# Optimization experiments

Measured on AMD Instinct MI355X. Metric: run time of the kernel, lower is better.

The kernel has to match this reference:

```python
import jax, jax.numpy as jnp
import numpy as np

S_MIN, S_MAX, ALPHA = 1, 5, 5.0
EPS = 1e-6


def _conv2d_same(x, k):
    # x: [B,1,H,W], k: [1,1,3,3], stride 1, padding 1
    return jax.lax.conv_general_dilated(x, k, (1, 1), ((1, 1), (1, 1)),
                                        dimension_numbers=('NCHW', 'OIHW', 'NCHW'))


def sobel_complexity(x):
    # compute_spatial_complexity_sobel: per-image min-max normalized gradient magnitude
    xg = x.mean(1, keepdims=True)  # [B,1,H,W]
    sx = jnp.array([[1, 0, -1], [2, 0, -2], [1, 0, -1]], x.dtype).reshape(1, 1, 3, 3)
    sy = jnp.array([[1, 2, 1], [0, 0, 0], [-1, -2, -1]], x.dtype).reshape(1, 1, 3, 3)
    gx = _conv2d_same(xg, sx)
    gy = _conv2d_same(xg, sy)
    mag = jnp.sqrt(gx ** 2 + gy ** 2 + EPS)
    mn = mag.min((2, 3), keepdims=True)
    mx = mag.max((2, 3), keepdims=True)
    rng = mx - mn
    c = jnp.where(rng > 0, (mag - mn) / (rng + EPS), jnp.zeros_like(mag))
    return c[:, 0]  # [B,H,W]


def adaptive_steps(m):
    # adaptive_step_from_complexity, fully vectorized
    B, H, W = m.shape
    avg = jnp.ones((1, 1, 3, 3), m.dtype) / 9.0
    lc = _conv2d_same(m[:, None], avg)[:, 0]  # [B,H,W] local complexity
    hm, wm = H // 2, W // 2
    rc = jnp.stack([m[:, :hm, :wm].mean((1, 2)), m[:, :hm, wm:].mean((1, 2)),
                    m[:, hm:, :wm].mean((1, 2)), m[:, hm:, wm:].mean((1, 2))], axis=1)  # [B,4]
    base = S_MAX - jax.nn.sigmoid(ALPHA * (rc - 0.5)) * (S_MAX - S_MIN)
    base = jnp.round(jnp.clip(base, S_MIN, S_MAX)).astype(jnp.int32)  # [B,4]
    adj = jnp.round(jax.nn.sigmoid(ALPHA * (lc - 0.5)) * 2.0 - 1.0).astype(jnp.int32)  # [B,H,W]
    return jnp.clip(base[:, :, None, None] + adj[:, None], S_MIN, S_MAX)  # [B,4,H,W]


def _visits_lr(step):
    # step: [B,R,L] int. Left-to-right adaptive-step traversal along last axis per row.
    # Returns float mask [B,R,L] of visited positions.
    B, R, L = step.shape
    s = jnp.maximum(step, 1)

    def body(j, _):
        valid = j < L                       # [B,R]
        jc = jnp.minimum(j, L - 1)
        st = jnp.take_along_axis(s, jc[:, :, None], -1)[:, :, 0]
        return jnp.where(valid, j + st, j), (jc, valid)

    _, (jcs, valids) = jax.lax.scan(body, jnp.zeros((B, R), jnp.int32), None, length=L)
    jcs = jnp.moveaxis(jcs, 0, -1)          # [B,R,L]
    valids = jnp.moveaxis(valids, 0, -1)    # [B,R,L]
    bi = jnp.arange(B)[:, None, None]
    ri = jnp.arange(R)[None, :, None]
    vis = jnp.zeros((B, R, L), jnp.float32).at[bi, ri, jcs].add(valids.astype(jnp.float32))
    return (vis > 0).astype(jnp.float32)


def _visits_rl(step):
    # Right-to-left traversal == left-to-right on the mirrored step map, mirrored back.
    return jnp.flip(_visits_lr(jnp.flip(step, -1)), -1)


def _forward(x):
    m = sobel_complexity(x)                 # [B,H,W]
    steps = adaptive_steps(m)               # [B,4,H,W]
    v0 = _visits_lr(steps[:, 0])            # rows, left->right
    v1 = _visits_rl(steps[:, 1])            # rows, right->left
    v2 = jnp.swapaxes(_visits_lr(jnp.swapaxes(steps[:, 2], 1, 2)), 1, 2)  # cols, top->down
    v3 = jnp.swapaxes(_visits_rl(jnp.swapaxes(steps[:, 3], 1, 2)), 1, 2)  # cols, bottom->up
    V = v0 + v1 + v2 + v3                   # [B,H,W] visit counts
    # DirectionalScan followed by DirectionalMerge: output = sum_d x*visit_d / (V + 1e-6)
    return x * (V / (V + 1e-6))[:, None]


def setup_inputs() -> dict:
    key = jax.random.key(0)
    x = jax.random.normal(key, (8, 96, 256, 256), dtype=jnp.float32)
    return {"x": x}


def reference(x):
    return _forward(x)
```

## Files before the change

### kernel.cpp

```cpp
#include <hip/hip_runtime.h>
#include <math.h>

#define BB 8
#define CC 96
#define HH 256
#define WW 256
#define HW (HH*WW)

typedef unsigned long long u64;

__global__ void k_init(unsigned* mn_u, unsigned* mx_u) {
    int t = threadIdx.x;
    if (t < BB) { mn_u[t] = 0x7f800000u; mx_u[t] = 0u; }
}

__global__ void k_mean(const float* __restrict__ x, float* __restrict__ m) {
    int i = blockIdx.x * blockDim.x + threadIdx.x;
    const int per = HW / 4;
    if (i >= BB * per) return;
    int b = i / per, hw4 = i % per;
    const float4* xb = reinterpret_cast<const float4*>(x) + (size_t)b * CC * per + hw4;
    double a0 = 0, a1 = 0, a2 = 0, a3 = 0;
    for (int c = 0; c < CC; ++c) {
        float4 v = xb[(size_t)c * per];
        a0 += (double)v.x; a1 += (double)v.y; a2 += (double)v.z; a3 += (double)v.w;
    }
    float4 o;
    o.x = (float)(a0 / 96.0); o.y = (float)(a1 / 96.0);
    o.z = (float)(a2 / 96.0); o.w = (float)(a3 / 96.0);
    reinterpret_cast<float4*>(m)[i] = o;
}

__global__ void k_sobel(const float* __restrict__ m, float* __restrict__ mag,
                        unsigned* mn_u, unsigned* mx_u) {
    int row = blockIdx.x;
    int b = row >> 8, h = row & 255, w = threadIdx.x;
    const float* mb = m + (size_t)b * HW;
    auto at = [&](int hh, int ww) -> float {
        if (hh < 0 || hh >= HH || ww < 0 || ww >= WW) return 0.0f;
        return mb[hh * WW + ww];
    };
    float a00 = at(h - 1, w - 1), a01 = at(h - 1, w), a02 = at(h - 1, w + 1);
    float a10 = at(h, w - 1),                         a12 = at(h, w + 1);
    float a20 = at(h + 1, w - 1), a21 = at(h + 1, w), a22 = at(h + 1, w + 1);
    float gx = a00 - a02 + 2.0f * a10 - 2.0f * a12 + a20 - a22;
    float gy = a00 + 2.0f * a01 + a02 - a20 - 2.0f * a21 - a22;
    float mg = sqrtf(gx * gx + gy * gy + 1e-6f);
    mag[row * WW + w] = mg;

    float lmn = mg, lmx = mg;
    for (int off = 32; off; off >>= 1) {
        lmn = fminf(lmn, __shfl_down(lmn, off));
        lmx = fmaxf(lmx, __shfl_down(lmx, off));
    }
    __shared__ float smn[4], smx[4];
    int wv = threadIdx.x >> 6, ln = threadIdx.x & 63;
    if (ln == 0) { smn[wv] = lmn; smx[wv] = lmx; }
    __syncthreads();
    if (threadIdx.x == 0) {
        float bmn = fminf(fminf(smn[0], smn[1]), fminf(smn[2], smn[3]));
        float bmx = fmaxf(fmaxf(smx[0], smx[1]), fmaxf(smx[2], smx[3]));
        atomicMin(&mn_u[b], __float_as_uint(bmn));
        atomicMax(&mx_u[b], __float_as_uint(bmx));
    }
}

__global__ void k_cnorm(const float* __restrict__ mag, const unsigned* __restrict__ mn_u,
                        const unsigned* __restrict__ mx_u, float* __restrict__ c,
                        float* __restrict__ part) {
    int row = blockIdx.x;
    int b = row >> 8, w = threadIdx.x;
    float mn = __uint_as_float(mn_u[b]);
    float mx = __uint_as_float(mx_u[b]);
    float rng = mx - mn;
    float mg = mag[row * WW + w];
    float cc = (rng > 0.0f) ? (mg - mn) / (rng + 1e-6f) : 0.0f;
    c[row * WW + w] = cc;

    float r = cc;
    for (int off = 32; off; off >>= 1) r += __shfl_down(r, off);
    __shared__ float s[4];
    int wv = threadIdx.x >> 6, ln = threadIdx.x & 63;
    if (ln == 0) s[wv] = r;
    __syncthreads();
    if (threadIdx.x == 0) {
        part[row * 2 + 0] = s[0] + s[1];
        part[row * 2 + 1] = s[2] + s[3];
    }
}

__global__ void k_base(const float* __restrict__ part, int* __restrict__ base) {
    int t = threadIdx.x;
    if (t >= 32) return;
    int b = t >> 2, q = t & 3;
    int hlo = (q >> 1) ? 128 : 0;
    int col = q & 1;
    double s = 0.0;
    for (int h = hlo; h < hlo + 128; ++h) s += (double)part[(b * HH + h) * 2 + col];
    float rc = (float)(s / 16384.0);
    float sig = 1.0f / (1.0f + expf(-5.0f * (rc - 0.5f)));
    float bs = 5.0f - sig * 4.0f;
    bs = fminf(fmaxf(bs, 1.0f), 5.0f);
    base[b * 4 + q] = (int)rintf(bs);
}

__global__ void k_adj(const float* __restrict__ c, signed char* __restrict__ adj) {
    int row = blockIdx.x;
    int b = row >> 8, h = row & 255, w = threadIdx.x;
    const float* cb = c + (size_t)b * HW;
    auto at = [&](int hh, int ww) -> float {
        if (hh < 0 || hh >= HH || ww < 0 || ww >= WW) return 0.0f;
        return cb[hh * WW + ww];
    };
    const float w9 = 1.0f / 9.0f;
    float acc = 0.0f;
    acc = fmaf(at(h - 1, w - 1), w9, acc);
    acc = fmaf(at(h - 1, w    ), w9, acc);
    acc = fmaf(at(h - 1, w + 1), w9, acc);
    acc = fmaf(at(h    , w - 1), w9, acc);
    acc = fmaf(at(h    , w    ), w9, acc);
    acc = fmaf(at(h    , w + 1), w9, acc);
    acc = fmaf(at(h + 1, w - 1), w9, acc);
    acc = fmaf(at(h + 1, w    ), w9, acc);
    acc = fmaf(at(h + 1, w + 1), w9, acc);
    float sg = 1.0f / (1.0f + expf(-5.0f * (acc - 0.5f)));
    adj[row * WW + w] = (signed char)(int)rintf(sg * 2.0f - 1.0f);
}

#define SETBIT(j) do { int _j = (j); \
    if (_j < 64) m0 |= 1ull << _j; \
    else if (_j < 128) m1 |= 1ull << (_j - 64); \
    else if (_j < 192) m2 |= 1ull << (_j - 128); \
    else m3 |= 1ull << (_j - 192); } while (0)

__global__ void k_trav(const signed char* __restrict__ adj, const int* __restrict__ base,
                       u64* __restrict__ masks) {
    int tid = blockIdx.x * blockDim.x + threadIdx.x;
    int dir = tid >> 11;
    int idx = tid & 2047;
    int b = idx >> 8, r = idx & 255;
    int bs = base[b * 4 + dir];
    const signed char* ab = adj + (size_t)b * HW;
    u64 m0 = 0, m1 = 0, m2 = 0, m3 = 0;
    if (dir == 0) {
        int j = 0;
        while (j < WW) {
            SETBIT(j);
            int st = bs + (int)ab[r * WW + j];
            st = st < 1 ? 1 : (st > 5 ? 5 : st);
            j += st;
        }
    } else if (dir == 1) {
        int j = WW - 1;
        while (j >= 0) {
            SETBIT(j);
            int st = bs + (int)ab[r * WW + j];
            st = st < 1 ? 1 : (st > 5 ? 5 : st);
            j -= st;
        }
    } else if (dir == 2) {
        int j = 0;
        while (j < HH) {
            SETBIT(j);
            int st = bs + (int)ab[j * WW + r];
            st = st < 1 ? 1 : (st > 5 ? 5 : st);
            j += st;
        }
    } else {
        int j = HH - 1;
        while (j >= 0) {
            SETBIT(j);
            int st = bs + (int)ab[j * WW + r];
            st = st < 1 ? 1 : (st > 5 ? 5 : st);
            j -= st;
        }
    }
    u64* o = masks + ((size_t)dir * BB * 256 + idx) * 4;
    o[0] = m0; o[1] = m1; o[2] = m2; o[3] = m3;
}

__global__ void k_scale(const u64* __restrict__ masks, float* __restrict__ scale) {
    int row = blockIdx.x;
    int b = row >> 8, h = row & 255, w = threadIdx.x;
    const u64* m0 = masks + (((size_t)0 * BB + b) * 256 + h) * 4;
    const u64* m1 = masks + (((size_t)1 * BB + b) * 256 + h) * 4;
    const u64* m2 = masks + (((size_t)2 * BB + b) * 256 + w) * 4;
    const u64* m3 = masks + (((size_t)3 * BB + b) * 256 + w) * 4;
    int v = (int)((m0[w >> 6] >> (w & 63)) & 1ull)
          + (int)((m1[w >> 6] >> (w & 63)) & 1ull)
          + (int)((m2[h >> 6] >> (h & 63)) & 1ull)
          + (int)((m3[h >> 6] >> (h & 63)) & 1ull);
    float fV = (float)v;
    scale[row * WW + w] = fV / (fV + 1e-6f);
}

__global__ void k_out(const float* __restrict__ x, const float* __restrict__ scale,
                      float* __restrict__ out) {
    const int total4 = BB * CC * HW / 4;
    const int per_img4 = CC * HW / 4;
    const int hw4n = HW / 4;
    const float4* x4 = reinterpret_cast<const float4*>(x);
    const float4* s4 = reinterpret_cast<const float4*>(scale);
    float4* o4 = reinterpret_cast<float4*>(out);
    for (int i = blockIdx.x * blockDim.x + threadIdx.x; i < total4;
         i += gridDim.x * blockDim.x) {
        int b = i / per_img4;
        int hw4 = i % hw4n;
        float4 sv = s4[b * hw4n + hw4];
        float4 xv = x4[i];
        float4 ov;
        ov.x = xv.x * sv.x; ov.y = xv.y * sv.y; ov.z = xv.z * sv.z; ov.w = xv.w * sv.w;
        o4[i] = ov;
    }
}

extern "C" void kernel_launch(void* const* d_in, const int* in_sizes, int n_in,
                              void* d_out, int out_size, void* d_ws, size_t ws_size,
                              hipStream_t stream) {
    const float* x = (const float*)d_in[0];
    float* out = (float*)d_out;
    char* ws = (char*)d_ws;

    float* m     = (float*)(ws);
    float* mag   = (float*)(ws + (size_t)2 * 1024 * 1024);
    float* c     = (float*)(ws + (size_t)4 * 1024 * 1024);
    float* scale = (float*)(ws + (size_t)6 * 1024 * 1024);
    signed char* adj = (signed char*)(ws + (size_t)8 * 1024 * 1024);
    u64* masks   = (u64*)(ws + (size_t)8 * 1024 * 1024 + 524288);
    float* part  = (float*)(ws + (size_t)8 * 1024 * 1024 + 524288 + 262144);
    unsigned* mn_u = (unsigned*)(ws + (size_t)8 * 1024 * 1024 + 524288 + 262144 + 16384);
    unsigned* mx_u = mn_u + 8;
    int* base = (int*)(mn_u + 16);

    k_init<<<1, 64, 0, stream>>>(mn_u, mx_u);
    k_mean<<<(BB * HW / 4 + 255) / 256, 256, 0, stream>>>(x, m);
    k_sobel<<<BB * HH, 256, 0, stream>>>(m, mag, mn_u, mx_u);
    k_cnorm<<<BB * HH, 256, 0, stream>>>(mag, mn_u, mx_u, c, part);
    k_base<<<1, 32, 0, stream>>>(part, base);
    k_adj<<<BB * HH, 256, 0, stream>>>(c, adj);
    k_trav<<<32, 256, 0, stream>>>(adj, base, masks);
    k_scale<<<BB * HH, 256, 0, stream>>>(masks, scale);
    k_out<<<4096, 256, 0, stream>>>(x, scale, out);
}
```

Baseline: 200.8 us.

## Fuse init, normalization, box filter and base-step kernels to cut launches

Folds the min/max init into the mean kernel and merges the normalization and box-filter kernels. The normalized complexity is now recomputed on the fly from the gradient magnitude instead of being stored and reloaded. The base-step computation moves into the traversal kernel as a per-block shared-memory reduction, and the mean loop gets an unroll pragma. This removes three launches and one intermediate buffer, at the cost of redundant divides per stencil tap. The mean kernel dominates the runtime, so the overall effect should be small.

New measurement: 188.2 us. 6.3% less time.

```diff
diff --git a/kernel.cpp b/kernel.cpp
--- a/kernel.cpp
+++ b/kernel.cpp
@@ -9,18 +9,19 @@
 
 typedef unsigned long long u64;
 
-__global__ void k_init(unsigned* mn_u, unsigned* mx_u) {
-    int t = threadIdx.x;
-    if (t < BB) { mn_u[t] = 0x7f800000u; mx_u[t] = 0u; }
-}
-
-__global__ void k_mean(const float* __restrict__ x, float* __restrict__ m) {
+__global__ void k_mean(const float* __restrict__ x, float* __restrict__ m,
+                       unsigned* __restrict__ mn_u, unsigned* __restrict__ mx_u) {
+    if (blockIdx.x == 0 && threadIdx.x < 2 * BB) {
+        if (threadIdx.x < BB) mn_u[threadIdx.x] = 0x7f800000u;
+        else                  mx_u[threadIdx.x - BB] = 0u;
+    }
     int i = blockIdx.x * blockDim.x + threadIdx.x;
     const int per = HW / 4;
     if (i >= BB * per) return;
     int b = i / per, hw4 = i % per;
     const float4* xb = reinterpret_cast<const float4*>(x) + (size_t)b * CC * per + hw4;
     double a0 = 0, a1 = 0, a2 = 0, a3 = 0;
+#pragma unroll 8
     for (int c = 0; c < CC; ++c) {
         float4 v = xb[(size_t)c * per];
         a0 += (double)v.x; a1 += (double)v.y; a2 += (double)v.z; a3 += (double)v.w;
@@ -65,17 +66,21 @@
     }
 }
 
-__global__ void k_cnorm(const float* __restrict__ mag, const unsigned* __restrict__ mn_u,
-                        const unsigned* __restrict__ mx_u, float* __restrict__ c,
-                        float* __restrict__ part) {
+__global__ void k_adjpart(const float* __restrict__ mag, const unsigned* __restrict__ mn_u,
+                          const unsigned* __restrict__ mx_u, signed char* __restrict__ adj,
+                          float* __restrict__ part) {
     int row = blockIdx.x;
-    int b = row >> 8, w = threadIdx.x;
+    int b = row >> 8, h = row & 255, w = threadIdx.x;
     float mn = __uint_as_float(mn_u[b]);
     float mx = __uint_as_float(mx_u[b]);
     float rng = mx - mn;
-    float mg = mag[row * WW + w];
-    float cc = (rng > 0.0f) ? (mg - mn) / (rng + 1e-6f) : 0.0f;
-    c[row * WW + w] = cc;
+    const float* gb = mag + (size_t)b * HW;
+    auto cat = [&](int hh, int ww) -> float {
+        if (hh < 0 || hh >= HH || ww < 0 || ww >= WW) return 0.0f;
+        float mg = gb[hh * WW + ww];
+        return (rng > 0.0f) ? (mg - mn) / (rng + 1e-6f) : 0.0f;
+    };
+    float cc = cat(h, w);
 
     float r = cc;
     for (int off = 32; off; off >>= 1) r += __shfl_down(r, off);
@@ -87,42 +92,18 @@
         part[row * 2 + 0] = s[0] + s[1];
         part[row * 2 + 1] = s[2] + s[3];
     }
-}
-
-__global__ void k_base(const float* __restrict__ part, int* __restrict__ base) {
-    int t = threadIdx.x;
-    if (t >= 32) return;
-    int b = t >> 2, q = t & 3;
-    int hlo = (q >> 1) ? 128 : 0;
-    int col = q & 1;
-    double s = 0.0;
-    for (int h = hlo; h < hlo + 128; ++h) s += (double)part[(b * HH + h) * 2 + col];
-    float rc = (float)(s / 16384.0);
-    float sig = 1.0f / (1.0f + expf(-5.0f * (rc - 0.5f)));
-    float bs = 5.0f - sig * 4.0f;
-    bs = fminf(fmaxf(bs, 1.0f), 5.0f);
-    base[b * 4 + q] = (int)rintf(bs);
-}
-
-__global__ void k_adj(const float* __restrict__ c, signed char* __restrict__ adj) {
-    int row = blockIdx.x;
-    int b = row >> 8, h = row & 255, w = threadIdx.x;
-    const float* cb = c + (size_t)b * HW;
-    auto at = [&](int hh, int ww) -> float {
-        if (hh < 0 || hh >= HH || ww < 0 || ww >= WW) return 0.0f;
-        return cb[hh * WW + ww];
-    };
+
     const float w9 = 1.0f / 9.0f;
     float acc = 0.0f;
-    acc = fmaf(at(h - 1, w - 1), w9, acc);
-    acc = fmaf(at(h - 1, w    ), w9, acc);
-    acc = fmaf(at(h - 1, w + 1), w9, acc);
-    acc = fmaf(at(h    , w - 1), w9, acc);
-    acc = fmaf(at(h    , w    ), w9, acc);
-    acc = fmaf(at(h    , w + 1), w9, acc);
-    acc = fmaf(at(h + 1, w - 1), w9, acc);
-    acc = fmaf(at(h + 1, w    ), w9, acc);
-    acc = fmaf(at(h + 1, w + 1), w9, acc);
+    acc = fmaf(cat(h - 1, w - 1), w9, acc);
+    acc = fmaf(cat(h - 1, w    ), w9, acc);
+    acc = fmaf(cat(h - 1, w + 1), w9, acc);
+    acc = fmaf(cat(h    , w - 1), w9, acc);
+    acc = fmaf(cc,               w9, acc);
+    acc = fmaf(cat(h    , w + 1), w9, acc);
+    acc = fmaf(cat(h + 1, w - 1), w9, acc);
+    acc = fmaf(cat(h + 1, w    ), w9, acc);
+    acc = fmaf(cat(h + 1, w + 1), w9, acc);
     float sg = 1.0f / (1.0f + expf(-5.0f * (acc - 0.5f)));
     adj[row * WW + w] = (signed char)(int)rintf(sg * 2.0f - 1.0f);
 }
@@ -133,13 +114,33 @@
     else if (_j < 192) m2 |= 1ull << (_j - 128); \
     else m3 |= 1ull << (_j - 192); } while (0)
 
-__global__ void k_trav(const signed char* __restrict__ adj, const int* __restrict__ base,
-                       u64* __restrict__ masks) {
-    int tid = blockIdx.x * blockDim.x + threadIdx.x;
-    int dir = tid >> 11;
-    int idx = tid & 2047;
-    int b = idx >> 8, r = idx & 255;
-    int bs = base[b * 4 + dir];
+__global__ void k_travbase(const signed char* __restrict__ adj, const float* __restrict__ part,
+                           u64* __restrict__ masks) {
+    int blk = blockIdx.x;
+    int dir = blk >> 3, b = blk & 7;
+    int t = threadIdx.x;
+
+    __shared__ double sd[128];
+    __shared__ int sbs;
+    int hlo = (dir >> 1) ? 128 : 0;
+    int col = dir & 1;
+    if (t < 128) sd[t] = (double)part[((b << 8) + hlo + t) * 2 + col];
+    __syncthreads();
+    for (int str = 64; str > 0; str >>= 1) {
+        if (t < str) sd[t] += sd[t + str];
+        __syncthreads();
+    }
+    if (t == 0) {
+        float rc = (float)(sd[0] / 16384.0);
+        float sig = 1.0f / (1.0f + expf(-5.0f * (rc - 0.5f)));
+        float bsf = 5.0f - sig * 4.0f;
+        bsf = fminf(fmaxf(bsf, 1.0f), 5.0f);
+        sbs = (int)rintf(bsf);
+    }
+    __syncthreads();
+    int bs = sbs;
+
+    int r = t;
     const signed char* ab = adj + (size_t)b * HW;
     u64 m0 = 0, m1 = 0, m2 = 0, m3 = 0;
     if (dir == 0) {
@@ -175,7 +176,7 @@
             j -= st;
         }
     }
-    u64* o = masks + ((size_t)dir * BB * 256 + idx) * 4;
+    u64* o = masks + ((size_t)dir * BB * 256 + (b << 8) + r) * 4;
     o[0] = m0; o[1] = m1; o[2] = m2; o[3] = m3;
 }
 
@@ -223,22 +224,17 @@
 
     float* m     = (float*)(ws);
     float* mag   = (float*)(ws + (size_t)2 * 1024 * 1024);
-    float* c     = (float*)(ws + (size_t)4 * 1024 * 1024);
-    float* scale = (float*)(ws + (size_t)6 * 1024 * 1024);
-    signed char* adj = (signed char*)(ws + (size_t)8 * 1024 * 1024);
-    u64* masks   = (u64*)(ws + (size_t)8 * 1024 * 1024 + 524288);
-    float* part  = (float*)(ws + (size_t)8 * 1024 * 1024 + 524288 + 262144);
-    unsigned* mn_u = (unsigned*)(ws + (size_t)8 * 1024 * 1024 + 524288 + 262144 + 16384);
+    float* scale = (float*)(ws + (size_t)4 * 1024 * 1024);
+    signed char* adj = (signed char*)(ws + (size_t)6 * 1024 * 1024);
+    u64* masks   = (u64*)(ws + (size_t)6 * 1024 * 1024 + 524288);
+    float* part  = (float*)(ws + (size_t)6 * 1024 * 1024 + 524288 + 262144);
+    unsigned* mn_u = (unsigned*)(ws + (size_t)6 * 1024 * 1024 + 524288 + 262144 + 16384);
     unsigned* mx_u = mn_u + 8;
-    int* base = (int*)(mn_u + 16);
-
-    k_init<<<1, 64, 0, stream>>>(mn_u, mx_u);
-    k_mean<<<(BB * HW / 4 + 255) / 256, 256, 0, stream>>>(x, m);
+
+    k_mean<<<(BB * HW / 4 + 255) / 256, 256, 0, stream>>>(x, m, mn_u, mx_u);
     k_sobel<<<BB * HH, 256, 0, stream>>>(m, mag, mn_u, mx_u);
-    k_cnorm<<<BB * HH, 256, 0, stream>>>(mag, mn_u, mx_u, c, part);
-    k_base<<<1, 32, 0, stream>>>(part, base);
-    k_adj<<<BB * HH, 256, 0, stream>>>(c, adj);
-    k_trav<<<32, 256, 0, stream>>>(adj, base, masks);
+    k_adjpart<<<BB * HH, 256, 0, stream>>>(mag, mn_u, mx_u, adj, part);
+    k_travbase<<<32, 256, 0, stream>>>(adj, part, masks);
     k_scale<<<BB * HH, 256, 0, stream>>>(masks, scale);
     k_out<<<4096, 256, 0, stream>>>(x, scale, out);
 }
```
